# Optimization experiments

Hardware: AMD Instinct MI355X
Metric: run time of the kernel (lower is better)

Reference implementation:

```python
import jax, jax.numpy as jnp
import numpy as np

DIM = 128
HEADS = 4
DIM_HEAD = 32
HIDDEN = HEADS * DIM_HEAD  # 128
SCALE = DIM_HEAD ** -0.5


def setup_inputs() -> dict:
    key = jax.random.key(0)
    k1, k2, k3, k4 = jax.random.split(key, 4)
    b, c, h, w = 2, DIM, 64, 64
    x = jax.random.normal(k1, (b, c, h, w), dtype=jnp.float32)
    # conv1x1 weights stored as [out_ch, in_ch] (kernel is 1x1)
    w_qkv = jax.random.normal(k2, (3 * HIDDEN, DIM), dtype=jnp.float32) * (DIM ** -0.5)
    w_out = jax.random.normal(k3, (DIM, HIDDEN), dtype=jnp.float32) * (HIDDEN ** -0.5)
    b_out = jax.random.normal(k4, (DIM,), dtype=jnp.float32) * 0.01
    return {"x": x, "w_qkv": w_qkv, "w_out": w_out, "b_out": b_out}


def reference(x, w_qkv, w_out, b_out):
    b, c, h, w = x.shape
    n = h * w
    xf = x.reshape(b, c, n)                                   # [b,c,n]
    qkv = jnp.einsum('oc,bcn->bon', w_qkv, xf)                # conv1x1, no bias
    q, k, v = jnp.split(qkv, 3, axis=1)                       # each [b,hidden,n]
    q = q.reshape(b, HEADS, DIM_HEAD, n) * SCALE
    k = k.reshape(b, HEADS, DIM_HEAD, n)
    v = v.reshape(b, HEADS, DIM_HEAD, n)
    sim = jnp.einsum('bhdi,bhdj->bhij', q, k)                 # [b,h,n,n]
    attn = jax.nn.softmax(sim, axis=-1)
    out = jnp.einsum('bhij,bhdj->bhdi', attn, v)              # [b,h,d,n]
    out = out.reshape(b, HIDDEN, n)
    out = jnp.einsum('oc,bcn->bon', w_out, out) + b_out[None, :, None]
    return out.reshape(b, c, h, w) + x
```

## Files before the change

kernel.cpp:

```cpp
#include <hip/hip_runtime.h>
#include <hip/hip_bf16.h>

typedef __hip_bfloat16 bf16;
typedef float    f32x16 __attribute__((ext_vector_type(16)));
typedef __bf16   bf16x8 __attribute__((ext_vector_type(8)));
typedef unsigned uint4v __attribute__((ext_vector_type(4)));
typedef int      i32x2  __attribute__((ext_vector_type(2)));

#define N_TOK 4096
#define SCALE_L2E 0.2550348952703927f

__device__ __forceinline__ bf16x8 ld8(const bf16* p) { return *(const bf16x8*)p; }
__device__ __forceinline__ unsigned pack2(float a, float b) {
    unsigned short ua = __builtin_bit_cast(unsigned short, (__bf16)a);
    unsigned short ub = __builtin_bit_cast(unsigned short, (__bf16)b);
    return (unsigned)ua | ((unsigned)ub << 16);
}
__device__ __forceinline__ unsigned short f2b(float f) {
    return __builtin_bit_cast(unsigned short, (__bf16)f);
}
__device__ __forceinline__ __bf16 us2bf(unsigned short u) {
    return __builtin_bit_cast(__bf16, u);
}
__device__ __forceinline__ bf16x8 ldw(const unsigned short* rowp) {
    uint2 lo = *(const uint2*)rowp;
    uint2 hi = *(const uint2*)(rowp + 4);
    uint4v u = {lo.x, lo.y, hi.x, hi.y};
    return __builtin_bit_cast(bf16x8, u);
}

__global__ void __launch_bounds__(256)
qkv_mfma(const float* __restrict__ x, const float* __restrict__ w,
         bf16* __restrict__ qt, bf16* __restrict__ kt, bf16* __restrict__ vt) {
    int tok0 = blockIdx.x * 32;
    int b    = blockIdx.y;
    int z    = blockIdx.z;
    __shared__ unsigned short xs[128][32];
    __shared__ unsigned short wl[128][132];
    {
        int c = threadIdx.x >> 1, hf = threadIdx.x & 1;
        const float4* x4 = (const float4*)(x + (size_t)b * (128 * N_TOK) +
                                           (size_t)c * N_TOK + tok0 + hf * 16);
        float4 a = x4[0], bb = x4[1], cc = x4[2], dd = x4[3];
        unsigned* dst = (unsigned*)&xs[c][hf * 16];
        dst[0] = pack2(a.x, a.y);   dst[1] = pack2(a.z, a.w);
        dst[2] = pack2(bb.x, bb.y); dst[3] = pack2(bb.z, bb.w);
        dst[4] = pack2(cc.x, cc.y); dst[5] = pack2(cc.z, cc.w);
        dst[6] = pack2(dd.x, dd.y); dst[7] = pack2(dd.z, dd.w);
    }
    {
        float sc = (z == 0) ? SCALE_L2E : 1.0f;
        const float4* wb4 = (const float4*)(w + (size_t)z * 128 * 128);
#pragma unroll
        for (int s = 0; s < 16; ++s) {
            int i4 = threadIdx.x + s * 256;
            int o  = i4 >> 5, c4 = (i4 & 31) * 4;
            float4 wv4 = wb4[i4];
            *(uint2*)&wl[o][c4] = make_uint2(pack2(wv4.x * sc, wv4.y * sc),
                                             pack2(wv4.z * sc, wv4.w * sc));
        }
    }
    __syncthreads();
    int lane = threadIdx.x & 63, wv = threadIdx.x >> 6;
    int i = lane & 31, hl = lane >> 5;

    bf16x8 xf[8], wf[8];
#pragma unroll
    for (int kb = 0; kb < 8; ++kb) {
        bf16x8 f;
#pragma unroll
        for (int e = 0; e < 8; ++e) f[e] = us2bf(xs[kb * 16 + hl * 8 + e][i]);
        xf[kb] = f;
        wf[kb] = ldw(&wl[wv * 32 + i][kb * 16 + hl * 8]);
    }

    f32x16 D;
#pragma unroll
    for (int r = 0; r < 16; ++r) D[r] = 0.f;

    if (z < 2) {
#pragma unroll
        for (int kb = 0; kb < 8; ++kb)
            D = __builtin_amdgcn_mfma_f32_32x32x16_bf16(xf[kb], wf[kb], D, 0, 0, 0);
        bf16* base = (z == 0) ? qt : kt;
        unsigned short* dst = (unsigned short*)(base + ((size_t)(b * 4 + wv) * N_TOK + tok0) * 32);
#pragma unroll
        for (int r = 0; r < 16; ++r) {
            int tr = (r & 3) + 8 * (r >> 2) + 4 * hl;
            dst[tr * 32 + i] = f2b(D[r]);
        }
    } else {
#pragma unroll
        for (int kb = 0; kb < 8; ++kb)
            D = __builtin_amdgcn_mfma_f32_32x32x16_bf16(wf[kb], xf[kb], D, 0, 0, 0);
        unsigned short* dst = (unsigned short*)(vt + (size_t)(b * 4 + wv) * (32 * N_TOK) + tok0);
#pragma unroll
        for (int r = 0; r < 16; ++r) {
            int dr = (r & 3) + 8 * (r >> 2) + 4 * hl;
            dst[(size_t)dr * N_TOK + i] = f2b(D[r]);
        }
    }
}

__global__ void __launch_bounds__(512)
attn_mfma(const bf16* __restrict__ qt, const bf16* __restrict__ kt,
          const bf16* __restrict__ vt, bf16* __restrict__ ao) {
    int bid = blockIdx.x;
    int swz = (bid & 7) * 32 + (bid >> 3);
    int bh  = swz >> 5;
    int g   = swz & 31;
    int tid  = threadIdx.x;
    int lane = tid & 63, wv = tid >> 6;
    int qtl  = wv >> 1;
    int kh   = wv & 1;
    int i    = lane & 31, hl = lane >> 5;

    __shared__ uint4v lds[2][512];
    __shared__ float  lsh[4][64];

    const bf16* qb = qt + (size_t)bh * (N_TOK * 32) + (size_t)(g * 128 + qtl * 32) * 32;
    const bf16* kb = kt + (size_t)bh * (N_TOK * 32);
    const bf16* vb = vt + (size_t)bh * (32 * N_TOK);

    bf16x8 q1 = ld8(qb + i * 32 + hl * 8);
    bf16x8 q2 = ld8(qb + i * 32 + 16 + hl * 8);

    bool isK = tid < 256;
    int  u   = isK ? tid : tid - 256;
    int kgoff = (((u >> 7) * 32) + (u & 31)) * 32 + ((u >> 6) & 1) * 16 + ((u >> 5) & 1) * 8;
    int vgoff = (u >> 3) * N_TOK + (u & 7) * 8;
    int ldst  = isK ? u : (256 + (u & 7) * 32 + (((u >> 3) + (u & 7)) & 31));

    f32x16 O, Z;
#pragma unroll
    for (int r = 0; r < 16; ++r) { O[r] = 0.f; Z[r] = 0.f; }
    float l = 0.f;

    int kidx1 = kh * 128 + lane;
    int kidx2 = kh * 128 + 64 + lane;
    int cc0 = kh * 4 + hl,     vidx1 = 256 + cc0 * 32 + ((i + cc0) & 31);
    int cc1 = kh * 4 + 2 + hl, vidx2 = 256 + cc1 * 32 + ((i + cc1) & 31);

    lds[0][ldst] = isK ? *(const uint4v*)(kb + kgoff) : *(const uint4v*)(vb + vgoff);
    __syncthreads();

    for (int c = 0; c < 64; ++c) {
        int bf = c & 1;
        uint4v nx;
        if (c < 63) {
            int j0 = (c + 1) * 64;
            nx = isK ? *(const uint4v*)(kb + (size_t)j0 * 32 + kgoff)
                     : *(const uint4v*)(vb + j0 + vgoff);
        }
        const uint4v* L = lds[bf];

        bf16x8 ka1 = __builtin_bit_cast(bf16x8, L[kidx1]);
        bf16x8 ka2 = __builtin_bit_cast(bf16x8, L[kidx2]);
        f32x16 S = __builtin_amdgcn_mfma_f32_32x32x16_bf16(ka1, q1, Z, 0, 0, 0);
        S = __builtin_amdgcn_mfma_f32_32x32x16_bf16(ka2, q2, S, 0, 0, 0);

        float p[16];
#pragma unroll
        for (int r = 0; r < 16; ++r) p[r] = __builtin_amdgcn_exp2f(S[r]);
        float s0 = (p[0] + p[1]) + (p[2] + p[3]);
        float s1 = (p[4] + p[5]) + (p[6] + p[7]);
        float s2 = (p[8] + p[9]) + (p[10] + p[11]);
        float s3 = (p[12] + p[13]) + (p[14] + p[15]);
        l += (s0 + s1) + (s2 + s3);

        unsigned pk0 = pack2(p[0], p[1]),   pk1 = pack2(p[2], p[3]);
        unsigned pk2 = pack2(p[4], p[5]),   pk3 = pack2(p[6], p[7]);
        unsigned pk4 = pack2(p[8], p[9]),   pk5 = pack2(p[10], p[11]);
        unsigned pk6 = pack2(p[12], p[13]), pk7 = pack2(p[14], p[15]);

        i32x2 t1 = __builtin_amdgcn_permlane32_swap((int)pk0, (int)pk2, false, false);
        i32x2 t2 = __builtin_amdgcn_permlane32_swap((int)pk1, (int)pk3, false, false);
        i32x2 t3 = __builtin_amdgcn_permlane32_swap((int)pk4, (int)pk6, false, false);
        i32x2 t4 = __builtin_amdgcn_permlane32_swap((int)pk5, (int)pk7, false, false);

        uint4v B1u = {(unsigned)t1.x, (unsigned)t2.x, (unsigned)t1.y, (unsigned)t2.y};
        uint4v B2u = {(unsigned)t3.x, (unsigned)t4.x, (unsigned)t3.y, (unsigned)t4.y};

        bf16x8 va1 = __builtin_bit_cast(bf16x8, L[vidx1]);
        bf16x8 va2 = __builtin_bit_cast(bf16x8, L[vidx2]);
        O = __builtin_amdgcn_mfma_f32_32x32x16_bf16(va1, __builtin_bit_cast(bf16x8, B1u), O, 0, 0, 0);
        O = __builtin_amdgcn_mfma_f32_32x32x16_bf16(va2, __builtin_bit_cast(bf16x8, B2u), O, 0, 0, 0);

        if (c < 63) lds[bf ^ 1][ldst] = nx;
        __syncthreads();
    }

    l += __shfl_xor(l, 32);
    float* fb = (float*)lds;
    if (kh == 1) {
#pragma unroll
        for (int r = 0; r < 16; ++r) fb[qtl * 1024 + r * 64 + lane] = O[r];
        lsh[qtl][lane] = l;
    }
    __syncthreads();
    if (kh == 0) {
        float lt  = l + lsh[qtl][lane];
        float inv = 1.f / lt;
        unsigned short* aop = (unsigned short*)(ao + (size_t)bh * (32 * N_TOK) + g * 128 + qtl * 32);
#pragma unroll
        for (int r = 0; r < 16; ++r) {
            float s = O[r] + fb[qtl * 1024 + r * 64 + lane];
            int d = (r & 3) + 8 * (r >> 2) + 4 * hl;
            aop[(size_t)d * N_TOK + i] = f2b(s * inv);
        }
    }
}

__global__ void __launch_bounds__(256)
out_mfma(const bf16* __restrict__ ao, const float* __restrict__ w,
         const float* __restrict__ bias, const float* __restrict__ x,
         float* __restrict__ out) {
    int tok0 = blockIdx.x * 32;
    int b    = blockIdx.y;
    __shared__ unsigned short as_[128][32];
    __shared__ unsigned short wl[128][132];
    {
        int c = threadIdx.x >> 1, hf = threadIdx.x & 1;
        const uint4v* src = (const uint4v*)(ao + (size_t)b * (128 * N_TOK) +
                                            (size_t)c * N_TOK + tok0 + hf * 16);
        uint4v v0 = src[0], v1 = src[1];
        uint4v* dst = (uint4v*)&as_[c][hf * 16];
        dst[0] = v0; dst[1] = v1;
    }
    {
        const float4* wb4 = (const float4*)w;
#pragma unroll
        for (int s = 0; s < 16; ++s) {
            int i4 = threadIdx.x + s * 256;
            int o  = i4 >> 5, c4 = (i4 & 31) * 4;
            float4 wv4 = wb4[i4];
            *(uint2*)&wl[o][c4] = make_uint2(pack2(wv4.x, wv4.y), pack2(wv4.z, wv4.w));
        }
    }
    __syncthreads();
    int lane = threadIdx.x & 63, wv = threadIdx.x >> 6;
    int i = lane & 31, hl = lane >> 5;

    bf16x8 af[8], wf[8];
#pragma unroll
    for (int kb = 0; kb < 8; ++kb) {
        bf16x8 f;
#pragma unroll
        for (int e = 0; e < 8; ++e) f[e] = us2bf(as_[kb * 16 + hl * 8 + e][i]);
        af[kb] = f;
        wf[kb] = ldw(&wl[wv * 32 + i][kb * 16 + hl * 8]);
    }

    f32x16 D;
#pragma unroll
    for (int r = 0; r < 16; ++r) D[r] = 0.f;
#pragma unroll
    for (int kb = 0; kb < 8; ++kb)
        D = __builtin_amdgcn_mfma_f32_32x32x16_bf16(wf[kb], af[kb], D, 0, 0, 0);

#pragma unroll
    for (int r = 0; r < 16; ++r) {
        int o_r = wv * 32 + (r & 3) + 8 * (r >> 2) + 4 * hl;
        size_t idx = ((size_t)b * 128 + o_r) * N_TOK + tok0 + i;
        out[idx] = D[r] + bias[o_r] + x[idx];
    }
}

extern "C" void kernel_launch(void* const* d_in, const int* in_sizes, int n_in,
                              void* d_out, int out_size, void* d_ws, size_t ws_size,
                              hipStream_t stream) {
    const float* x     = (const float*)d_in[0];
    const float* w_qkv = (const float*)d_in[1];
    const float* w_out = (const float*)d_in[2];
    const float* b_out = (const float*)d_in[3];
    float* out = (float*)d_out;

    bf16* qt = (bf16*)d_ws;
    bf16* kt = qt + (size_t)8 * N_TOK * 32;
    bf16* vt = kt + (size_t)8 * N_TOK * 32;
    bf16* ao = vt + (size_t)8 * N_TOK * 32;

    qkv_mfma <<<dim3(128, 2, 3), 256, 0, stream>>>(x, w_qkv, qt, kt, vt);
    attn_mfma<<<dim3(256), 512, 0, stream>>>(qt, kt, vt, ao);
    out_mfma <<<dim3(128, 2), 256, 0, stream>>>(ao, w_out, b_out, x, out);
}
```

Before: 112.4 us.

## Halve attention block size, process two KV chunks per sync, sum rows via MFMA

The attention kernel moves from 512-thread blocks handling 128 queries to 256-thread blocks handling 64 queries, which doubles the grid and drops the block-index swizzle. Each loop iteration now loads and computes two 64-key chunks from a 4-deep LDS ring, so half as many barriers are needed. The softmax row sum is no longer a scalar VALU reduction; it comes from extra MFMAs against a vector of ones. The trade-offs are more register pressure, twice the K/V reloading per query (each block covers fewer queries), and four extra MFMAs per iteration.

```diff
diff --git a/kernel.cpp b/kernel.cpp
--- a/kernel.cpp
+++ b/kernel.cpp
@@ -102,106 +102,141 @@
     }
 }
 
-__global__ void __launch_bounds__(512)
+__global__ void __launch_bounds__(256)
 attn_mfma(const bf16* __restrict__ qt, const bf16* __restrict__ kt,
           const bf16* __restrict__ vt, bf16* __restrict__ ao) {
-    int bid = blockIdx.x;
-    int swz = (bid & 7) * 32 + (bid >> 3);
-    int bh  = swz >> 5;
-    int g   = swz & 31;
+    int bid  = blockIdx.x;
+    int bh   = bid & 7;
+    int g    = bid >> 3;
     int tid  = threadIdx.x;
     int lane = tid & 63, wv = tid >> 6;
     int qtl  = wv >> 1;
     int kh   = wv & 1;
     int i    = lane & 31, hl = lane >> 5;
 
-    __shared__ uint4v lds[2][512];
-    __shared__ float  lsh[4][64];
-
-    const bf16* qb = qt + (size_t)bh * (N_TOK * 32) + (size_t)(g * 128 + qtl * 32) * 32;
+    __shared__ uint4v lds[4][512];
+
+    const bf16* qb = qt + (size_t)bh * (N_TOK * 32) + (size_t)(g * 64 + qtl * 32) * 32;
     const bf16* kb = kt + (size_t)bh * (N_TOK * 32);
     const bf16* vb = vt + (size_t)bh * (32 * N_TOK);
 
     bf16x8 q1 = ld8(qb + i * 32 + hl * 8);
     bf16x8 q2 = ld8(qb + i * 32 + 16 + hl * 8);
 
-    bool isK = tid < 256;
-    int  u   = isK ? tid : tid - 256;
-    int kgoff = (((u >> 7) * 32) + (u & 31)) * 32 + ((u >> 6) & 1) * 16 + ((u >> 5) & 1) * 8;
+    bf16x8 ones;
+#pragma unroll
+    for (int e = 0; e < 8; ++e) ones[e] = us2bf(0x3F80);
+
+    f32x16 O, Ol, Z;
+#pragma unroll
+    for (int r = 0; r < 16; ++r) { O[r] = 0.f; Ol[r] = 0.f; Z[r] = 0.f; }
+
+    int u = tid;
+    int kgoff = ((u >> 7) * 32 + (u & 31)) * 32 + ((u >> 6) & 1) * 16 + ((u >> 5) & 1) * 8;
     int vgoff = (u >> 3) * N_TOK + (u & 7) * 8;
-    int ldst  = isK ? u : (256 + (u & 7) * 32 + (((u >> 3) + (u & 7)) & 31));
-
-    f32x16 O, Z;
-#pragma unroll
-    for (int r = 0; r < 16; ++r) { O[r] = 0.f; Z[r] = 0.f; }
-    float l = 0.f;
-
-    int kidx1 = kh * 128 + lane;
-    int kidx2 = kh * 128 + 64 + lane;
-    int cc0 = kh * 4 + hl,     vidx1 = 256 + cc0 * 32 + ((i + cc0) & 31);
-    int cc1 = kh * 4 + 2 + hl, vidx2 = 256 + cc1 * 32 + ((i + cc1) & 31);
-
-    lds[0][ldst] = isK ? *(const uint4v*)(kb + kgoff) : *(const uint4v*)(vb + vgoff);
+    int ldstK = u;
+    int ldstV = 256 + (u & 7) * 32 + (((u >> 3) + (u & 7)) & 31);
+
+    int kidx1 = kh * 128 + lane, kidx2 = kidx1 + 64;
+    int cA = kh * 4 + hl,     vidx1 = 256 + cA * 32 + ((i + cA) & 31);
+    int cB = kh * 4 + 2 + hl, vidx2 = 256 + cB * 32 + ((i + cB) & 31);
+
+    lds[0][ldstK] = *(const uint4v*)(kb + kgoff);
+    lds[0][ldstV] = *(const uint4v*)(vb + vgoff);
+    lds[1][ldstK] = *(const uint4v*)(kb + (size_t)64 * 32 + kgoff);
+    lds[1][ldstV] = *(const uint4v*)(vb + 64 + vgoff);
     __syncthreads();
 
-    for (int c = 0; c < 64; ++c) {
-        int bf = c & 1;
-        uint4v nx;
-        if (c < 63) {
-            int j0 = (c + 1) * 64;
-            nx = isK ? *(const uint4v*)(kb + (size_t)j0 * 32 + kgoff)
-                     : *(const uint4v*)(vb + j0 + vgoff);
-        }
-        const uint4v* L = lds[bf];
-
-        bf16x8 ka1 = __builtin_bit_cast(bf16x8, L[kidx1]);
-        bf16x8 ka2 = __builtin_bit_cast(bf16x8, L[kidx2]);
-        f32x16 S = __builtin_amdgcn_mfma_f32_32x32x16_bf16(ka1, q1, Z, 0, 0, 0);
-        S = __builtin_amdgcn_mfma_f32_32x32x16_bf16(ka2, q2, S, 0, 0, 0);
-
-        float p[16];
-#pragma unroll
-        for (int r = 0; r < 16; ++r) p[r] = __builtin_amdgcn_exp2f(S[r]);
-        float s0 = (p[0] + p[1]) + (p[2] + p[3]);
-        float s1 = (p[4] + p[5]) + (p[6] + p[7]);
-        float s2 = (p[8] + p[9]) + (p[10] + p[11]);
-        float s3 = (p[12] + p[13]) + (p[14] + p[15]);
-        l += (s0 + s1) + (s2 + s3);
-
-        unsigned pk0 = pack2(p[0], p[1]),   pk1 = pack2(p[2], p[3]);
-        unsigned pk2 = pack2(p[4], p[5]),   pk3 = pack2(p[6], p[7]);
-        unsigned pk4 = pack2(p[8], p[9]),   pk5 = pack2(p[10], p[11]);
-        unsigned pk6 = pack2(p[12], p[13]), pk7 = pack2(p[14], p[15]);
-
-        i32x2 t1 = __builtin_amdgcn_permlane32_swap((int)pk0, (int)pk2, false, false);
-        i32x2 t2 = __builtin_amdgcn_permlane32_swap((int)pk1, (int)pk3, false, false);
-        i32x2 t3 = __builtin_amdgcn_permlane32_swap((int)pk4, (int)pk6, false, false);
-        i32x2 t4 = __builtin_amdgcn_permlane32_swap((int)pk5, (int)pk7, false, false);
-
-        uint4v B1u = {(unsigned)t1.x, (unsigned)t2.x, (unsigned)t1.y, (unsigned)t2.y};
-        uint4v B2u = {(unsigned)t3.x, (unsigned)t4.x, (unsigned)t3.y, (unsigned)t4.y};
-
-        bf16x8 va1 = __builtin_bit_cast(bf16x8, L[vidx1]);
-        bf16x8 va2 = __builtin_bit_cast(bf16x8, L[vidx2]);
-        O = __builtin_amdgcn_mfma_f32_32x32x16_bf16(va1, __builtin_bit_cast(bf16x8, B1u), O, 0, 0, 0);
-        O = __builtin_amdgcn_mfma_f32_32x32x16_bf16(va2, __builtin_bit_cast(bf16x8, B2u), O, 0, 0, 0);
-
-        if (c < 63) lds[bf ^ 1][ldst] = nx;
+    for (int t = 0; t < 32; ++t) {
+        uint4v nk0, nv0, nk1, nv1;
+        if (t < 31) {
+            size_t j0 = (size_t)(2 * t + 2) * 64;
+            nk0 = *(const uint4v*)(kb + j0 * 32 + kgoff);
+            nv0 = *(const uint4v*)(vb + j0 + vgoff);
+            nk1 = *(const uint4v*)(kb + (j0 + 64) * 32 + kgoff);
+            nv1 = *(const uint4v*)(vb + (j0 + 64) + vgoff);
+        }
+        const uint4v* LA = lds[(2 * t) & 3];
+        const uint4v* LB = lds[(2 * t + 1) & 3];
+
+        bf16x8 kaA1 = __builtin_bit_cast(bf16x8, LA[kidx1]);
+        bf16x8 kaA2 = __builtin_bit_cast(bf16x8, LA[kidx2]);
+        f32x16 SA = __builtin_amdgcn_mfma_f32_32x32x16_bf16(kaA1, q1, Z, 0, 0, 0);
+        SA = __builtin_amdgcn_mfma_f32_32x32x16_bf16(kaA2, q2, SA, 0, 0, 0);
+        bf16x8 kaB1 = __builtin_bit_cast(bf16x8, LB[kidx1]);
+        bf16x8 kaB2 = __builtin_bit_cast(bf16x8, LB[kidx2]);
+        f32x16 SB = __builtin_amdgcn_mfma_f32_32x32x16_bf16(kaB1, q1, Z, 0, 0, 0);
+        SB = __builtin_amdgcn_mfma_f32_32x32x16_bf16(kaB2, q2, SB, 0, 0, 0);
+
+        bf16x8 vaA1 = __builtin_bit_cast(bf16x8, LA[vidx1]);
+        bf16x8 vaA2 = __builtin_bit_cast(bf16x8, LA[vidx2]);
+        bf16x8 vaB1 = __builtin_bit_cast(bf16x8, LB[vidx1]);
+        bf16x8 vaB2 = __builtin_bit_cast(bf16x8, LB[vidx2]);
+
+        {
+            float p[16];
+#pragma unroll
+            for (int r = 0; r < 16; ++r) p[r] = __builtin_amdgcn_exp2f(SA[r]);
+            unsigned pk0 = pack2(p[0], p[1]),   pk1 = pack2(p[2], p[3]);
+            unsigned pk2 = pack2(p[4], p[5]),   pk3 = pack2(p[6], p[7]);
+            unsigned pk4 = pack2(p[8], p[9]),   pk5 = pack2(p[10], p[11]);
+            unsigned pk6 = pack2(p[12], p[13]), pk7 = pack2(p[14], p[15]);
+            i32x2 t1 = __builtin_amdgcn_permlane32_swap((int)pk0, (int)pk2, false, false);
+            i32x2 t2 = __builtin_amdgcn_permlane32_swap((int)pk1, (int)pk3, false, false);
+            i32x2 t3 = __builtin_amdgcn_permlane32_swap((int)pk4, (int)pk6, false, false);
+            i32x2 t4 = __builtin_amdgcn_permlane32_swap((int)pk5, (int)pk7, false, false);
+            uint4v B1u = {(unsigned)t1.x, (unsigned)t2.x, (unsigned)t1.y, (unsigned)t2.y};
+            uint4v B2u = {(unsigned)t3.x, (unsigned)t4.x, (unsigned)t3.y, (unsigned)t4.y};
+            bf16x8 B1 = __builtin_bit_cast(bf16x8, B1u);
+            bf16x8 B2 = __builtin_bit_cast(bf16x8, B2u);
+            O  = __builtin_amdgcn_mfma_f32_32x32x16_bf16(vaA1, B1, O, 0, 0, 0);
+            O  = __builtin_amdgcn_mfma_f32_32x32x16_bf16(vaA2, B2, O, 0, 0, 0);
+            Ol = __builtin_amdgcn_mfma_f32_32x32x16_bf16(ones, B1, Ol, 0, 0, 0);
+            Ol = __builtin_amdgcn_mfma_f32_32x32x16_bf16(ones, B2, Ol, 0, 0, 0);
+        }
+        {
+            float p[16];
+#pragma unroll
+            for (int r = 0; r < 16; ++r) p[r] = __builtin_amdgcn_exp2f(SB[r]);
+            unsigned pk0 = pack2(p[0], p[1]),   pk1 = pack2(p[2], p[3]);
+            unsigned pk2 = pack2(p[4], p[5]),   pk3 = pack2(p[6], p[7]);
+            unsigned pk4 = pack2(p[8], p[9]),   pk5 = pack2(p[10], p[11]);
+            unsigned pk6 = pack2(p[12], p[13]), pk7 = pack2(p[14], p[15]);
+            i32x2 t1 = __builtin_amdgcn_permlane32_swap((int)pk0, (int)pk2, false, false);
+            i32x2 t2 = __builtin_amdgcn_permlane32_swap((int)pk1, (int)pk3, false, false);
+            i32x2 t3 = __builtin_amdgcn_permlane32_swap((int)pk4, (int)pk6, false, false);
+            i32x2 t4 = __builtin_amdgcn_permlane32_swap((int)pk5, (int)pk7, false, false);
+            uint4v B1u = {(unsigned)t1.x, (unsigned)t2.x, (unsigned)t1.y, (unsigned)t2.y};
+            uint4v B2u = {(unsigned)t3.x, (unsigned)t4.x, (unsigned)t3.y, (unsigned)t4.y};
+            bf16x8 B1 = __builtin_bit_cast(bf16x8, B1u);
+            bf16x8 B2 = __builtin_bit_cast(bf16x8, B2u);
+            O  = __builtin_amdgcn_mfma_f32_32x32x16_bf16(vaB1, B1, O, 0, 0, 0);
+            O  = __builtin_amdgcn_mfma_f32_32x32x16_bf16(vaB2, B2, O, 0, 0, 0);
+            Ol = __builtin_amdgcn_mfma_f32_32x32x16_bf16(ones, B1, Ol, 0, 0, 0);
+            Ol = __builtin_amdgcn_mfma_f32_32x32x16_bf16(ones, B2, Ol, 0, 0, 0);
+        }
+
+        if (t < 31) {
+            lds[(2 * t + 2) & 3][ldstK] = nk0;
+            lds[(2 * t + 2) & 3][ldstV] = nv0;
+            lds[(2 * t + 3) & 3][ldstK] = nk1;
+            lds[(2 * t + 3) & 3][ldstV] = nv1;
+        }
         __syncthreads();
     }
 
-    l += __shfl_xor(l, 32);
     float* fb = (float*)lds;
+    float l = Ol[0];
     if (kh == 1) {
 #pragma unroll
         for (int r = 0; r < 16; ++r) fb[qtl * 1024 + r * 64 + lane] = O[r];
-        lsh[qtl][lane] = l;
+        fb[2048 + qtl * 64 + lane] = l;
     }
     __syncthreads();
     if (kh == 0) {
-        float lt  = l + lsh[qtl][lane];
+        float lt  = l + fb[2048 + qtl * 64 + lane];
         float inv = 1.f / lt;
-        unsigned short* aop = (unsigned short*)(ao + (size_t)bh * (32 * N_TOK) + g * 128 + qtl * 32);
+        unsigned short* aop = (unsigned short*)(ao + (size_t)bh * (32 * N_TOK) + g * 64 + qtl * 32);
 #pragma unroll
         for (int r = 0; r < 16; ++r) {
             float s = O[r] + fb[qtl * 1024 + r * 64 + lane];
@@ -281,6 +316,6 @@
     bf16* ao = vt + (size_t)8 * N_TOK * 32;
 
     qkv_mfma <<<dim3(128, 2, 3), 256, 0, stream>>>(x, w_qkv, qt, kt, vt);
-    attn_mfma<<<dim3(256), 512, 0, stream>>>(qt, kt, vt, ao);
+    attn_mfma<<<dim3(512), 256, 0, stream>>>(qt, kt, vt, ao);
     out_mfma <<<dim3(128, 2), 256, 0, stream>>>(ao, w_out, b_out, x, out);
 }
```

After: 106.8 us. -5.0%, faster.
